# Kernel tuning notes

Measured on AMD Instinct MI355X. Metric: run time of the kernel, lower is better.

Reference implementation:

```python
import jax, jax.numpy as jnp
import numpy as np

EPS = 1e-10

def _mlp(x, W1, b1, W2, b2):
    # Linear -> ReLU -> Linear (matches _MultiLayerPercep)
    return jnp.maximum(x @ W1 + b1, 0.0) @ W2 + b2

def setup_inputs() -> dict:
    key = jax.random.key(0)
    ks = jax.random.split(key, 24)
    B, P, Q, P2, D = 512, 100, 40, 40, 64
    Nu, Ni, Nr = 100000, 100000, 6

    def lin(k, fi, fo):
        kw, kb = jax.random.split(k)
        s = 1.0 / np.sqrt(fi)
        return (jax.random.uniform(kw, (fi, fo), jnp.float32, -s, s),
                jax.random.uniform(kb, (fo,), jnp.float32, -s, s))

    uids = jax.random.randint(ks[0], (B,), 0, Nu)
    u_item_pad = jnp.stack([jax.random.randint(ks[1], (B, P), 0, Ni),
                            jax.random.randint(ks[2], (B, P), 0, Nr)], axis=-1)
    u_user_pad = jax.random.randint(ks[3], (B, Q), 0, Nu)
    u_user_item_pad = jnp.stack([jax.random.randint(ks[4], (B, Q, P2), 0, Ni),
                                 jax.random.randint(ks[5], (B, Q, P2), 0, Nr)], axis=-1)

    user_table = jax.random.normal(ks[6], (Nu, D), jnp.float32) * 0.1
    item_table = jax.random.normal(ks[7], (Ni, D), jnp.float32) * 0.1
    rate_table = jax.random.normal(ks[8], (Nr, D), jnp.float32) * 0.1

    gv_W1, gv_b1 = lin(ks[9], 2 * D, D)
    gv_W2, gv_b2 = lin(ks[10], D, D)
    atti_W1, atti_b1 = lin(ks[11], 2 * D, D)
    atti_W2, atti_b2 = lin(ks[12], D, 1)
    agg_W, agg_b = lin(ks[13], D, D)
    attu_W1, attu_b1 = lin(ks[14], 2 * D, D)
    attu_W2, attu_b2 = lin(ks[15], D, 1)
    aggn_W, aggn_b = lin(ks[16], D, D)
    cm_W1, cm_b1 = lin(ks[17], 2 * D, D)
    cm_W2, cm_b2 = lin(ks[18], D, D)
    cm_W3, cm_b3 = lin(ks[19], D, D)

    return dict(uids=uids, u_item_pad=u_item_pad, u_user_pad=u_user_pad,
                u_user_item_pad=u_user_item_pad,
                user_table=user_table, item_table=item_table, rate_table=rate_table,
                gv_W1=gv_W1, gv_b1=gv_b1, gv_W2=gv_W2, gv_b2=gv_b2,
                atti_W1=atti_W1, atti_b1=atti_b1, atti_W2=atti_W2, atti_b2=atti_b2,
                agg_W=agg_W, agg_b=agg_b,
                attu_W1=attu_W1, attu_b1=attu_b1, attu_W2=attu_W2, attu_b2=attu_b2,
                aggn_W=aggn_W, aggn_b=aggn_b,
                cm_W1=cm_W1, cm_b1=cm_b1, cm_W2=cm_W2, cm_b2=cm_b2, cm_W3=cm_W3, cm_b3=cm_b3)

def reference(uids, u_item_pad, u_user_pad, u_user_item_pad,
              user_table, item_table, rate_table,
              gv_W1, gv_b1, gv_W2, gv_b2,
              atti_W1, atti_b1, atti_W2, atti_b2,
              agg_W, agg_b,
              attu_W1, attu_b1, attu_W2, attu_b2,
              aggn_W, aggn_b,
              cm_W1, cm_b1, cm_W2, cm_b2, cm_W3, cm_b3):
    f32 = jnp.float32

    # ---- item aggregation branch ----
    q_a = item_table[u_item_pad[:, :, 0]]                      # [B,P,D]
    mask_u = (u_item_pad[:, :, 0] > 0).astype(f32)             # [B,P]
    er = rate_table[u_item_pad[:, :, 1]]                       # [B,P,D]
    x_ia = _mlp(jnp.concatenate([q_a, er], -1), gv_W1, gv_b1, gv_W2, gv_b2)
    p_i = mask_u[..., None] * user_table[uids][:, None, :]     # [B,P,D]
    alpha = _mlp(jnp.concatenate([x_ia, p_i], -1), atti_W1, atti_b1, atti_W2, atti_b2)[..., 0]
    alpha = jnp.exp(alpha) * mask_u
    alpha = alpha / (jnp.sum(alpha, axis=1, keepdims=True) + EPS)
    h_iI = jnp.maximum(jnp.sum(alpha[..., None] * x_ia, axis=1) @ agg_W + agg_b, 0.0)  # [B,D]

    # ---- social branch: per-neighbor item aggregation ----
    q_a_s = item_table[u_user_item_pad[:, :, :, 0]]            # [B,Q,P2,D]
    mask_s = (u_user_item_pad[:, :, :, 0] > 0).astype(f32)     # [B,Q,P2]
    er_s = rate_table[u_user_item_pad[:, :, :, 1]]
    x_ia_s = _mlp(jnp.concatenate([q_a_s, er_s], -1), gv_W1, gv_b1, gv_W2, gv_b2)
    nbr_emb = user_table[u_user_pad]                           # [B,Q,D]
    p_i_s = mask_s[..., None] * nbr_emb[:, :, None, :]
    alpha_s = _mlp(jnp.concatenate([x_ia_s, p_i_s], -1), atti_W1, atti_b1, atti_W2, atti_b2)[..., 0]
    alpha_s = jnp.exp(alpha_s) * mask_s
    alpha_s = alpha_s / (jnp.sum(alpha_s, axis=2, keepdims=True) + EPS)
    h_oI = jnp.maximum(jnp.sum(alpha_s[..., None] * x_ia_s, axis=2) @ agg_W + agg_b, 0.0)  # [B,Q,D]

    # ---- social attention over neighbors ----
    beta = _mlp(jnp.concatenate([h_oI, nbr_emb], -1), attu_W1, attu_b1, attu_W2, attu_b2)[..., 0]
    mask_su = (u_user_pad > 0).astype(f32)
    beta = jnp.exp(beta) * mask_su
    beta = beta / (jnp.sum(beta, axis=1, keepdims=True) + EPS)
    h_iS = jnp.maximum(jnp.sum(beta[..., None] * h_oI, axis=1) @ aggn_W + aggn_b, 0.0)  # [B,D]

    # ---- combine ----
    h = jnp.maximum(jnp.concatenate([h_iI, h_iS], -1) @ cm_W1 + cm_b1, 0.0)
    h = jnp.maximum(h @ cm_W2 + cm_b2, 0.0)
    h = jnp.maximum(h @ cm_W3 + cm_b3, 0.0)
    return h
```

## Files before the change

kernel.cpp:

```cpp
#include <hip/hip_runtime.h>
#include <math.h>

#define EPSV 1e-10f

typedef _Float16 f16x8 __attribute__((ext_vector_type(8)));
typedef _Float16 f16x4 __attribute__((ext_vector_type(4)));
typedef float f32x4 __attribute__((ext_vector_type(4)));

#define OFF_W1T  0
#define OFF_W2T  16384
#define OFF_M2T  24576
#define OFF_U    32768
#define OFF_B1   33792
#define OFF_R1   34048
#define OFF_V    36864
#define SMEM_SZ  40960

__device__ __forceinline__ f16x8 cvt_f16x8(const float4 a, const float4 b) {
  f16x8 h;
  h[0] = (_Float16)a.x; h[1] = (_Float16)a.y; h[2] = (_Float16)a.z; h[3] = (_Float16)a.w;
  h[4] = (_Float16)b.x; h[5] = (_Float16)b.y; h[6] = (_Float16)b.z; h[7] = (_Float16)b.w;
  return h;
}

__global__ __launch_bounds__(256, 3) void agg_kernel(
    const int nIblk,
    const int* __restrict__ idsS, const int* __restrict__ uidS,
    const int* __restrict__ idsI, const int* __restrict__ uidI,
    const float* __restrict__ user_table, const float* __restrict__ item_table,
    const float* __restrict__ rate_table,
    const float* __restrict__ gv_W1, const float* __restrict__ gv_b1,
    const float* __restrict__ gv_W2, const float* __restrict__ gv_b2,
    const float* __restrict__ atti_W1, const float* __restrict__ atti_b1,
    const float* __restrict__ atti_W2, const float* __restrict__ atti_b2,
    const float* __restrict__ agg_W, const float* __restrict__ agg_b,
    float* __restrict__ outS, float* __restrict__ outI) {
  __shared__ __align__(16) char smem[SMEM_SZ];
  const int tid = threadIdx.x;
  const int wave = tid >> 6, lane = tid & 63;
  const int quad = lane >> 4, mrow = lane & 15;

  const bool isS = (int)blockIdx.x >= nIblk;
  const int NG = isS ? 16 : 4;
  const int P = isS ? 40 : 100;
  const int nGrp = isS ? 4 : 1;
  const int tpg = isS ? 3 : 8;
  const int nIdx = nGrp * tpg;
  const int* __restrict__ ids = isS ? idsS : idsI;
  const int* __restrict__ uidp = isS ? uidS : uidI;
  float* __restrict__ out = isS ? outS : outI;
  const int gbase = isS ? ((int)blockIdx.x - nIblk) * 16 : (int)blockIdx.x * 4;

  float* sV = (float*)(smem + OFF_V);
  char* smXw = smem + OFF_W1T + wave * 4096;
  float* csW = (float*)smXw;

  {
    float* uS = (float*)(smem + OFF_U);
    float* AU = (float*)(smem + OFF_W1T);
    for (int t = tid; t < NG * 64; t += 256) {
      const int g = t >> 6, f = t & 63;
      uS[t] = user_table[(size_t)uidp[gbase + g] * 64 + f];
    }
    for (int o = tid; o < 1024; o += 256) {
      const int k = o >> 4, fb = o & 15;
      const float4 v = ((const float4*)(atti_W1 + (64 + k) * 64))[fb];
      const float* vp = (const float*)&v;
#pragma unroll
      for (int c = 0; c < 4; ++c) {
        const int j = fb * 4 + c;
        AU[j * 64 + (((k >> 2) ^ (j & 15)) << 2) + (k & 3)] = vp[c];
      }
    }
  }
  __syncthreads();
  {
    const float4* u4 = (const float4*)(smem + OFF_U);
    const float4* a4 = (const float4*)(smem + OFF_W1T);
    for (int t = tid; t < NG * 64; t += 256) {
      const int g = t >> 6, j = t & 63;
      float s = 0.f;
#pragma unroll 4
      for (int kb = 0; kb < 16; ++kb) {
        const float4 uu = u4[g * 16 + kb];
        const float4 aa = a4[j * 16 + (kb ^ (j & 15))];
        s += uu.x * aa.x + uu.y * aa.y + uu.z * aa.z + uu.w * aa.w;
      }
      sV[t] = s;
    }
  }
  __syncthreads();
  {
    for (int o = tid; o < 1024; o += 256) {
      const int k = o >> 4, fb = o & 15;
      const float4 v = ((const float4*)(gv_W1 + k * 64))[fb];
      const float* vp = (const float*)&v;
#pragma unroll
      for (int c = 0; c < 4; ++c) {
        const int n = fb * 4 + c;
        *(_Float16*)(smem + OFF_W1T + n * 256 + ((((k >> 3) ^ (n & 7))) << 4) +
                     ((k & 7) << 1)) = (_Float16)vp[c];
      }
    }
    for (int o = tid; o < 1024; o += 256) {
      const int h = o >> 4, fb = o & 15;
      const float4 v = ((const float4*)(gv_W2 + h * 64))[fb];
      const float* vp = (const float*)&v;
#pragma unroll
      for (int c = 0; c < 4; ++c) {
        const int n = fb * 4 + c;
        *(_Float16*)(smem + OFF_W2T + n * 128 + ((((h >> 3) ^ (n & 7))) << 4) +
                     ((h & 7) << 1)) = (_Float16)vp[c];
      }
    }
    {
      float* sR1 = (float*)(smem + OFF_R1);
      for (int o = tid; o < 384; o += 256) {
        const int r = o >> 6, n = o & 63;
        float s = 0.f;
#pragma unroll 8
        for (int k = 0; k < 64; ++k)
          s = fmaf(rate_table[r * 64 + k], gv_W1[(64 + k) * 64 + n], s);
        sR1[r * 68 + n] = s;
      }
    }
    if (tid < 16) ((float4*)(smem + OFF_B1))[tid] = ((const float4*)gv_b1)[tid];
    float* sCstP = (float*)(smem + OFF_U);
    const int n = tid & 63, jh = tid >> 6;
    float p = 0.f;
#pragma unroll 4
    for (int jj = 0; jj < 16; ++jj) {
      const int j = jh * 16 + jj;
      p = fmaf(gv_b2[j], atti_W1[j * 64 + n], p);
    }
    sCstP[jh * 64 + n] = p;
  }
  float b2v[4], aw2v[4];
#pragma unroll
  for (int nt = 0; nt < 4; ++nt) {
    b2v[nt] = gv_b2[nt * 16 + mrow];
    aw2v[nt] = atti_W2[nt * 16 + mrow];
  }
  const float ab2 = atti_b2[0];

  const int nIdxM1 = nIdx - 1;
  int2 idreg;
  float4 pf[4];
  float pm;
  int rid;
  auto load_ids = [&](int idx) __attribute__((always_inline)) {
    const int ic = idx < nIdxM1 ? idx : nIdxM1;
    const int gq = isS ? (ic * 11) >> 5 : (ic >> 3);
    const int tt = ic - gq * tpg;
    const int it = tt * 16 + mrow;
    int2 pr = make_int2(0, 0);
    if (it < P) {
      const int g2 = gbase + wave + 4 * gq;
      pr = ((const int2*)ids)[(size_t)g2 * P + it];
    }
    idreg = pr;
  };
  auto issue_gather = [&]() __attribute__((always_inline)) {
    const int iid = idreg.x;
    rid = idreg.y;
    pm = iid > 0 ? 1.f : 0.f;
    const float* ib = item_table + (size_t)iid * 64 + quad * 8;
    pf[0] = ((const float4*)ib)[0];
    pf[1] = ((const float4*)ib)[1];
    pf[2] = ((const float4*)(ib + 32))[0];
    pf[3] = ((const float4*)(ib + 32))[1];
  };
  load_ids(0); issue_gather();
  load_ids(1);
  __syncthreads();
  float cstv[4];
  {
    f16x8 aM[2];
#pragma unroll
    for (int ks = 0; ks < 2; ++ks) {
      f16x8 t;
#pragma unroll
      for (int j = 0; j < 8; ++j)
        t[j] = (_Float16)atti_W1[(ks * 32 + quad * 8 + j) * 64 + (wave * 16 + mrow)];
      aM[ks] = t;
    }
#pragma unroll
    for (int ht = 0; ht < 4; ++ht) {
      f32x4 c = {0.f, 0.f, 0.f, 0.f};
#pragma unroll
      for (int ks = 0; ks < 2; ++ks) {
        const float* s = gv_W2 + (ht * 16 + mrow) * 64 + ks * 32 + quad * 8;
        f16x8 b;
#pragma unroll
        for (int j = 0; j < 8; ++j) b[j] = (_Float16)s[j];
        c = __builtin_amdgcn_mfma_f32_16x16x32_f16(aM[ks], b, c, 0, 0, 0);
      }
      const int h = ht * 16 + mrow;
#pragma unroll
      for (int rg = 0; rg < 4; ++rg) {
        const int n3 = wave * 16 + quad * 4 + rg;
        *(_Float16*)(smem + OFF_M2T + n3 * 128 + ((((h >> 3) ^ (n3 & 7))) << 4) +
                     ((h & 7) << 1)) = (_Float16)c[rg];
      }
    }
    const float* sCstP = (const float*)(smem + OFF_U);
#pragma unroll
    for (int nt = 0; nt < 4; ++nt) {
      const int n = nt * 16 + mrow;
      cstv[nt] = atti_b1[n] + sCstP[n] + sCstP[64 + n] + sCstP[128 + n] +
                 sCstP[192 + n];
    }
  }
  __syncthreads();

  f16x8 aW[4][2];
#pragma unroll
  for (int nt = 0; nt < 4; ++nt) {
#pragma unroll
    for (int ks = 0; ks < 2; ++ks)
      aW[nt][ks] = *(const f16x8*)(smem + OFF_W1T + (nt * 16 + mrow) * 256 +
                                   (((ks * 4 + quad) ^ (mrow & 7)) << 4));
  }
  __syncthreads();

  const float* sR1 = (const float*)(smem + OFF_R1);
  float vv[4], pnum[4], pden = 0.f;
  for (int idx = 0; idx < nIdx; ++idx) {
    const int gq = isS ? (idx * 11) >> 5 : (idx >> 3);
    const int tt = idx - gq * tpg;
    const int g = wave + 4 * gq;
    if (tt == 0) {
#pragma unroll
      for (int nt = 0; nt < 4; ++nt) {
        vv[nt] = sV[g * 64 + nt * 16 + mrow];
        pnum[nt] = 0.f;
      }
      pden = 0.f;
    }
    f16x8 bIn0 = cvt_f16x8(pf[0], pf[1]);
    f16x8 bIn1 = cvt_f16x8(pf[2], pf[3]);
    const float mcur = pm;
    const int ridcur = rid;
    issue_gather();
    load_ids(idx + 2);
#pragma unroll
    for (int nt = 0; nt < 4; ++nt) {
      f32x4 c = {0.f, 0.f, 0.f, 0.f};
      c = __builtin_amdgcn_mfma_f32_16x16x32_f16(aW[nt][0], bIn0, c, 0, 0, 0);
      c = __builtin_amdgcn_mfma_f32_16x16x32_f16(aW[nt][1], bIn1, c, 0, 0, 0);
      const float4 b1q = *(const float4*)(smem + OFF_B1 + nt * 64 + quad * 16);
      const float* b1p = (const float*)&b1q;
      const float4 r1q = *(const float4*)(sR1 + ridcur * 68 + nt * 16 + quad * 4);
      const float* r1p = (const float*)&r1q;
      f16x4 hv;
#pragma unroll
      for (int rg = 0; rg < 4; ++rg)
        hv[rg] = (_Float16)fmaxf(c[rg] + b1p[rg] + r1p[rg], 0.f);
      *(f16x4*)(smXw + mrow * 256 +
                (((nt * 2 + (quad >> 1)) ^ (mrow & 7)) << 4) +
                ((quad & 1) << 3)) = hv;
    }
    f16x8 a2[2];
#pragma unroll
    for (int ks = 0; ks < 2; ++ks)
      a2[ks] = *(const f16x8*)(smXw + mrow * 256 +
                               (((ks * 4 + quad) ^ (mrow & 7)) << 4));
    float mk[4];
#pragma unroll
    for (int rg = 0; rg < 4; ++rg) mk[rg] = __shfl(mcur, quad * 4 + rg);
    float tl[4] = {0.f, 0.f, 0.f, 0.f};
#pragma unroll
    for (int nt = 0; nt < 4; ++nt) {
      f32x4 d = {0.f, 0.f, 0.f, 0.f};
#pragma unroll
      for (int ks = 0; ks < 2; ++ks) {
        const f16x8 bM = *(const f16x8*)(smem + OFF_M2T + (nt * 16 + mrow) * 128 +
                                         (((ks * 4 + quad) ^ (mrow & 7)) << 4));
        d = __builtin_amdgcn_mfma_f32_16x16x32_f16(a2[ks], bM, d, 0, 0, 0);
      }
#pragma unroll
      for (int rg = 0; rg < 4; ++rg) {
        const float hh = fmaxf(d[rg] + cstv[nt] + mk[rg] * vv[nt], 0.f);
        tl[rg] = fmaf(hh, aw2v[nt], tl[rg]);
      }
    }
    float e[4];
#pragma unroll
    for (int rg = 0; rg < 4; ++rg) {
      float t = tl[rg];
      t += __shfl_xor(t, 1); t += __shfl_xor(t, 2);
      t += __shfl_xor(t, 4); t += __shfl_xor(t, 8);
      e[rg] = __expf(t + ab2) * mk[rg];
      pden += e[rg];
    }
#pragma unroll
    for (int nt = 0; nt < 4; ++nt) {
      f32x4 c = {0.f, 0.f, 0.f, 0.f};
#pragma unroll
      for (int ks = 0; ks < 2; ++ks) {
        const f16x8 bW = *(const f16x8*)(smem + OFF_W2T + (nt * 16 + mrow) * 128 +
                                         (((ks * 4 + quad) ^ (mrow & 7)) << 4));
        c = __builtin_amdgcn_mfma_f32_16x16x32_f16(a2[ks], bW, c, 0, 0, 0);
      }
      pnum[nt] = fmaf(e[0], c[0], pnum[nt]);
      pnum[nt] = fmaf(e[1], c[1], pnum[nt]);
      pnum[nt] = fmaf(e[2], c[2], pnum[nt]);
      pnum[nt] = fmaf(e[3], c[3], pnum[nt]);
    }
    if (tt == tpg - 1) {
      float dsum = pden;
      dsum += __shfl_xor(dsum, 16); dsum += __shfl_xor(dsum, 32);
      const float rd = 1.f / (dsum + EPSV);
#pragma unroll
      for (int nt = 0; nt < 4; ++nt) {
        float s = pnum[nt];
        s += __shfl_xor(s, 16); s += __shfl_xor(s, 32);
        if (quad == 0) csW[nt * 16 + mrow] = (s + b2v[nt] * dsum) * rd;
      }
      float acc = agg_b[lane];
#pragma unroll 8
      for (int k = 0; k < 64; ++k) acc = fmaf(csW[k], agg_W[k * 64 + lane], acc);
      out[(size_t)(gbase + g) * 64 + lane] = fmaxf(acc, 0.f);
    }
  }
}

#define S2_W1T 0
#define S2_X   17408
#define S2_E   26112
#define S2_MSK 26240
#define S2_HB  26368
#define S2_SZ  27904

__global__ __launch_bounds__(128, 2) void stage2_kernel(
    const int* __restrict__ u_user_pad, const float* __restrict__ user_table,
    const float* __restrict__ hoI, const float* __restrict__ hiI,
    const float* __restrict__ attu_W1, const float* __restrict__ attu_b1,
    const float* __restrict__ attu_W2, const float* __restrict__ attu_b2,
    const float* __restrict__ aggn_W, const float* __restrict__ aggn_b,
    const float* __restrict__ cm_W1, const float* __restrict__ cm_b1,
    const float* __restrict__ cm_W2, const float* __restrict__ cm_b2,
    const float* __restrict__ cm_W3, const float* __restrict__ cm_b3,
    float* __restrict__ out) {
  __shared__ __align__(16) char smem[S2_SZ];
  const int tid = threadIdx.x;
  const int wave = tid >> 6, lane = tid & 63;
  const int quad = lane >> 4, mrow = lane & 15;
  const int b = (int)blockIdx.x * 2 + wave;

  char* sW1 = smem + S2_W1T;
  char* sXw = smem + S2_X + wave * 4352;
  float* sE = (float*)(smem + S2_E) + wave * 16;
  float* sM = (float*)(smem + S2_MSK) + wave * 16;
  float* sB = (float*)(smem + S2_HB) + wave * 192;

  for (int o = tid; o < 2048; o += 128) {
    const int k = o >> 4, fb = o & 15;
    const float4 v = ((const float4*)(attu_W1 + k * 64))[fb];
    const float* vp = (const float*)&v;
#pragma unroll
    for (int c = 0; c < 4; ++c) {
      const int n = fb * 4 + c;
      *(_Float16*)(sW1 + n * 272 + ((k >> 3) << 4) + ((k & 7) << 1)) = (_Float16)vp[c];
    }
  }
  float b1v[4], w2v[4];
#pragma unroll
  for (int nt = 0; nt < 4; ++nt) {
    b1v[nt] = attu_b1[nt * 16 + mrow];
    w2v[nt] = attu_W2[nt * 16 + mrow];
  }
  const float b2s = attu_b2[0];

  float4 pa[4], pb[4];
  float msk[4];
  auto pf = [&](int tt) __attribute__((always_inline)) {
#pragma unroll
    for (int k = 0; k < 4; ++k) {
      const int u = lane + (k << 6);
      const int r = u >> 4, bb = u & 15;
      const int q = tt * 16 + r;
      const int qc = q < 40 ? q : 39;
      int uid = 0;
      float m = 0.f;
      if (q < 40) {
        uid = u_user_pad[b * 40 + q];
        m = uid > 0 ? 1.f : 0.f;
      }
      msk[k] = m;
      const float* src = (bb < 8)
                             ? hoI + ((size_t)b * 40 + qc) * 64 + bb * 8
                             : user_table + (size_t)uid * 64 + (bb - 8) * 8;
      pa[k] = ((const float4*)src)[0];
      pb[k] = ((const float4*)src)[1];
    }
  };
  pf(0);
  __syncthreads();

  float numer = 0.f, pden = 0.f;
  for (int tt = 0; tt < 3; ++tt) {
#pragma unroll
    for (int k = 0; k < 4; ++k) {
      const int u = lane + (k << 6);
      const int r = u >> 4, bb = u & 15;
      *(f16x8*)(sXw + r * 272 + (bb << 4)) = cvt_f16x8(pa[k], pb[k]);
      if (bb == 0) sM[r] = msk[k];
    }
    if (tt < 2) pf(tt + 1);
    f16x8 a[4];
#pragma unroll
    for (int ks = 0; ks < 4; ++ks)
      a[ks] = *(const f16x8*)(sXw + mrow * 272 + ((ks * 4 + quad) << 4));
    float mk[4];
#pragma unroll
    for (int rg = 0; rg < 4; ++rg) mk[rg] = sM[quad * 4 + rg];
    float tl[4] = {0.f, 0.f, 0.f, 0.f};
#pragma unroll
    for (int nt = 0; nt < 4; ++nt) {
      f32x4 d = {0.f, 0.f, 0.f, 0.f};
      const int n = nt * 16 + mrow;
#pragma unroll
      for (int ks = 0; ks < 4; ++ks) {
        const f16x8 bW = *(const f16x8*)(sW1 + n * 272 + ((ks * 4 + quad) << 4));
        d = __builtin_amdgcn_mfma_f32_16x16x32_f16(a[ks], bW, d, 0, 0, 0);
      }
#pragma unroll
      for (int rg = 0; rg < 4; ++rg) {
        const float h = fmaxf(d[rg] + b1v[nt], 0.f);
        tl[rg] = fmaf(h, w2v[nt], tl[rg]);
      }
    }
    float e[4];
#pragma unroll
    for (int rg = 0; rg < 4; ++rg) {
      float t = tl[rg];
      t += __shfl_xor(t, 1); t += __shfl_xor(t, 2);
      t += __shfl_xor(t, 4); t += __shfl_xor(t, 8);
      e[rg] = __expf(t + b2s) * mk[rg];
      pden += e[rg];
    }
    if (mrow == 0) {
#pragma unroll
      for (int rg = 0; rg < 4; ++rg) sE[quad * 4 + rg] = e[rg];
    }
#pragma unroll 4
    for (int r = 0; r < 16; ++r) {
      const float er = sE[r];
      const float xv = (float)*(const _Float16*)(sXw + r * 272 + ((lane >> 3) << 4) +
                                                 ((lane & 7) << 1));
      numer = fmaf(er, xv, numer);
    }
  }
  pden += __shfl_xor(pden, 16);
  pden += __shfl_xor(pden, 32);
  const float hagg = numer / (pden + EPSV);

  sB[128 + lane] = hagg;
  sB[lane] = hiI[(size_t)b * 64 + lane];
  float acc = aggn_b[lane];
#pragma unroll 8
  for (int k = 0; k < 64; ++k) acc = fmaf(sB[128 + k], aggn_W[k * 64 + lane], acc);
  sB[64 + lane] = fmaxf(acc, 0.f);
  float c1 = cm_b1[lane];
#pragma unroll 8
  for (int k = 0; k < 128; ++k) c1 = fmaf(sB[k], cm_W1[k * 64 + lane], c1);
  sB[128 + lane] = fmaxf(c1, 0.f);
  float c2 = cm_b2[lane];
#pragma unroll 8
  for (int k = 0; k < 64; ++k) c2 = fmaf(sB[128 + k], cm_W2[k * 64 + lane], c2);
  sB[lane] = fmaxf(c2, 0.f);
  float c3 = cm_b3[lane];
#pragma unroll 8
  for (int k = 0; k < 64; ++k) c3 = fmaf(sB[k], cm_W3[k * 64 + lane], c3);
  out[(size_t)b * 64 + lane] = fmaxf(c3, 0.f);
}

extern "C" void kernel_launch(void* const* d_in, const int* in_sizes, int n_in,
                              void* d_out, int out_size, void* d_ws, size_t ws_size,
                              hipStream_t stream) {
  const int* uids = (const int*)d_in[0];
  const int* u_item_pad = (const int*)d_in[1];
  const int* u_user_pad = (const int*)d_in[2];
  const int* u_user_item_pad = (const int*)d_in[3];
  const float* user_table = (const float*)d_in[4];
  const float* item_table = (const float*)d_in[5];
  const float* rate_table = (const float*)d_in[6];
  const float* gv_W1 = (const float*)d_in[7];
  const float* gv_b1 = (const float*)d_in[8];
  const float* gv_W2 = (const float*)d_in[9];
  const float* gv_b2 = (const float*)d_in[10];
  const float* atti_W1 = (const float*)d_in[11];
  const float* atti_b1 = (const float*)d_in[12];
  const float* atti_W2 = (const float*)d_in[13];
  const float* atti_b2 = (const float*)d_in[14];
  const float* agg_W = (const float*)d_in[15];
  const float* agg_b = (const float*)d_in[16];
  const float* attu_W1 = (const float*)d_in[17];
  const float* attu_b1 = (const float*)d_in[18];
  const float* attu_W2 = (const float*)d_in[19];
  const float* attu_b2 = (const float*)d_in[20];
  const float* aggn_W = (const float*)d_in[21];
  const float* aggn_b = (const float*)d_in[22];
  const float* cm_W1 = (const float*)d_in[23];
  const float* cm_b1 = (const float*)d_in[24];
  const float* cm_W2 = (const float*)d_in[25];
  const float* cm_b2 = (const float*)d_in[26];
  const float* cm_W3 = (const float*)d_in[27];
  const float* cm_b3 = (const float*)d_in[28];
  float* out = (float*)d_out;

  float* hoI = (float*)d_ws;
  float* hiI = hoI + (size_t)512 * 40 * 64;

  agg_kernel<<<128 + 1280, 256, 0, stream>>>(
      128, u_user_item_pad, u_user_pad, u_item_pad, uids,
      user_table, item_table, rate_table,
      gv_W1, gv_b1, gv_W2, gv_b2,
      atti_W1, atti_b1, atti_W2, atti_b2,
      agg_W, agg_b, hoI, hiI);
  stage2_kernel<<<256, 128, 0, stream>>>(u_user_pad, user_table, hoI, hiI,
                                         attu_W1, attu_b1, attu_W2, attu_b2,
                                         aggn_W, aggn_b,
                                         cm_W1, cm_b1, cm_W2, cm_b2, cm_W3, cm_b3,
                                         out);
}
```

Baseline: 268.9 us.

## Software-pipeline the per-wave MLP loop with double-buffered LDS slots

The per-index loop body is split into two lambdas. Stage1 converts gathered inputs, runs the first gv MLP layer and writes the hidden tile to LDS. Stage2 runs the attention MLP, the exp weighting and the aggregation. A two-slot LDS buffer per wave lets stage1 of the next index run before stage2 of the current one, so MFMA chains and gathers from different indices can interleave for more ILP. The compact W1 layout uses a 128-byte row stride, and the AU scratch moves to its own offset so the double buffer fits. The cost is more register pressure and a changed order of id prefetches.

```diff
diff --git a/kernel.cpp b/kernel.cpp
--- a/kernel.cpp
+++ b/kernel.cpp
@@ -8,6 +8,7 @@
 typedef float f32x4 __attribute__((ext_vector_type(4)));
 
 #define OFF_W1T  0
+#define OFF_AU   16384
 #define OFF_W2T  16384
 #define OFF_M2T  24576
 #define OFF_U    32768
@@ -52,12 +53,11 @@
   const int gbase = isS ? ((int)blockIdx.x - nIblk) * 16 : (int)blockIdx.x * 4;
 
   float* sV = (float*)(smem + OFF_V);
-  char* smXw = smem + OFF_W1T + wave * 4096;
-  float* csW = (float*)smXw;
+  char* smXw = smem + wave * 4096;
 
   {
     float* uS = (float*)(smem + OFF_U);
-    float* AU = (float*)(smem + OFF_W1T);
+    float* AU = (float*)(smem + OFF_AU);
     for (int t = tid; t < NG * 64; t += 256) {
       const int g = t >> 6, f = t & 63;
       uS[t] = user_table[(size_t)uidp[gbase + g] * 64 + f];
@@ -76,7 +76,7 @@
   __syncthreads();
   {
     const float4* u4 = (const float4*)(smem + OFF_U);
-    const float4* a4 = (const float4*)(smem + OFF_W1T);
+    const float4* a4 = (const float4*)(smem + OFF_AU);
     for (int t = tid; t < NG * 64; t += 256) {
       const int g = t >> 6, j = t & 63;
       float s = 0.f;
@@ -98,7 +98,7 @@
 #pragma unroll
       for (int c = 0; c < 4; ++c) {
         const int n = fb * 4 + c;
-        *(_Float16*)(smem + OFF_W1T + n * 256 + ((((k >> 3) ^ (n & 7))) << 4) +
+        *(_Float16*)(smem + OFF_W1T + n * 128 + ((((k >> 3) ^ (n & 7))) << 4) +
                      ((k & 7) << 1)) = (_Float16)vp[c];
       }
     }
@@ -218,31 +218,21 @@
   for (int nt = 0; nt < 4; ++nt) {
 #pragma unroll
     for (int ks = 0; ks < 2; ++ks)
-      aW[nt][ks] = *(const f16x8*)(smem + OFF_W1T + (nt * 16 + mrow) * 256 +
+      aW[nt][ks] = *(const f16x8*)(smem + OFF_W1T + (nt * 16 + mrow) * 128 +
                                    (((ks * 4 + quad) ^ (mrow & 7)) << 4));
   }
   __syncthreads();
 
   const float* sR1 = (const float*)(smem + OFF_R1);
   float vv[4], pnum[4], pden = 0.f;
-  for (int idx = 0; idx < nIdx; ++idx) {
-    const int gq = isS ? (idx * 11) >> 5 : (idx >> 3);
-    const int tt = idx - gq * tpg;
-    const int g = wave + 4 * gq;
-    if (tt == 0) {
-#pragma unroll
-      for (int nt = 0; nt < 4; ++nt) {
-        vv[nt] = sV[g * 64 + nt * 16 + mrow];
-        pnum[nt] = 0.f;
-      }
-      pden = 0.f;
-    }
+
+  auto stage1 = [&](const int par, float& mS) __attribute__((always_inline)) {
     f16x8 bIn0 = cvt_f16x8(pf[0], pf[1]);
     f16x8 bIn1 = cvt_f16x8(pf[2], pf[3]);
-    const float mcur = pm;
+    mS = pm;
     const int ridcur = rid;
     issue_gather();
-    load_ids(idx + 2);
+    char* slot = smXw + (par << 11);
 #pragma unroll
     for (int nt = 0; nt < 4; ++nt) {
       f32x4 c = {0.f, 0.f, 0.f, 0.f};
@@ -256,18 +246,34 @@
 #pragma unroll
       for (int rg = 0; rg < 4; ++rg)
         hv[rg] = (_Float16)fmaxf(c[rg] + b1p[rg] + r1p[rg], 0.f);
-      *(f16x4*)(smXw + mrow * 256 +
+      *(f16x4*)(slot + mrow * 128 +
                 (((nt * 2 + (quad >> 1)) ^ (mrow & 7)) << 4) +
                 ((quad & 1) << 3)) = hv;
     }
+  };
+
+  auto stage2 = [&](const int idx, const int par, const float mS)
+      __attribute__((always_inline)) {
+    const int gq = isS ? (idx * 11) >> 5 : (idx >> 3);
+    const int tt = idx - gq * tpg;
+    const int g = wave + 4 * gq;
+    if (tt == 0) {
+#pragma unroll
+      for (int nt = 0; nt < 4; ++nt) {
+        vv[nt] = sV[g * 64 + nt * 16 + mrow];
+        pnum[nt] = 0.f;
+      }
+      pden = 0.f;
+    }
+    char* slot = smXw + (par << 11);
     f16x8 a2[2];
 #pragma unroll
     for (int ks = 0; ks < 2; ++ks)
-      a2[ks] = *(const f16x8*)(smXw + mrow * 256 +
+      a2[ks] = *(const f16x8*)(slot + mrow * 128 +
                                (((ks * 4 + quad) ^ (mrow & 7)) << 4));
     float mk[4];
 #pragma unroll
-    for (int rg = 0; rg < 4; ++rg) mk[rg] = __shfl(mcur, quad * 4 + rg);
+    for (int rg = 0; rg < 4; ++rg) mk[rg] = __shfl(mS, quad * 4 + rg);
     float tl[4] = {0.f, 0.f, 0.f, 0.f};
 #pragma unroll
     for (int nt = 0; nt < 4; ++nt) {
@@ -308,6 +314,7 @@
       pnum[nt] = fmaf(e[3], c[3], pnum[nt]);
     }
     if (tt == tpg - 1) {
+      float* csW = (float*)slot;
       float dsum = pden;
       dsum += __shfl_xor(dsum, 16); dsum += __shfl_xor(dsum, 32);
       const float rd = 1.f / (dsum + EPSV);
@@ -322,6 +329,21 @@
       for (int k = 0; k < 64; ++k) acc = fmaf(csW[k], agg_W[k * 64 + lane], acc);
       out[(size_t)(gbase + g) * 64 + lane] = fmaxf(acc, 0.f);
     }
+  };
+
+  float mA, mB;
+  load_ids(2);
+  stage1(0, mA);
+  load_ids(3);
+  for (int idx = 0; idx < nIdx; idx += 2) {
+    stage1(1, mB);
+    load_ids(idx + 3);
+    stage2(idx, 0, mA);
+    if (idx + 2 < nIdx) {
+      stage1(0, mA);
+      load_ids(idx + 4);
+    }
+    stage2(idx + 1, 1, mB);
   }
 }
 
```

Result: no change. 266.8 us (-0.8%).
